# Kernel tuning notes

Hardware: AMD Instinct MI355X
Metric: run time of the kernel (lower is better)

Reference implementation:

```python
import jax, jax.numpy as jnp
import numpy as np

N_FFT = 128
HOP = 32            # fft_stride
WIN_LEN = 512       # window_length
STRIDE = 128        # MPF stride
FS = 2000.0
BANDS = [(0.0, 100.0), (100.0, 200.0), (200.0, 300.0), (300.0, 500.0), (500.0, 750.0), (750.0, 1000.0)]
FRAME_SIZE = WIN_LEN // HOP   # 16 STFT frames per MPF window
FRAME_STEP = STRIDE // HOP    # 4


def _freq_masks():
    freqs = np.fft.rfftfreq(N_FFT, d=1.0 / FS)  # (F,) Hz
    m = np.stack([(freqs > lo) & (freqs <= hi) for lo, hi in BANDS]).astype(np.float32)  # (K, F)
    return jnp.asarray(m)


def setup_inputs() -> dict:
    key = jax.random.key(0)
    return {"inputs": jax.random.normal(key, (8, 16, 32768), dtype=jnp.float32)}


def reference(inputs) -> jnp.ndarray:
    # inputs: (B, C, T)
    B, C, T = inputs.shape
    window = jnp.hanning(N_FFT).astype(inputs.dtype)  # symmetric hann == torch periodic=False
    wnorm = jnp.linalg.norm(window)

    # --- channelwise STFT (center=False, onesided) ---
    n_frames = 1 + (T - N_FFT) // HOP
    fidx = np.arange(n_frames)[:, None] * HOP + np.arange(N_FFT)[None, :]  # (n_frames, N_FFT)
    frames = inputs[..., fidx] * window                                    # (B, C, n_frames, N_FFT)
    stft = jnp.fft.rfft(frames, axis=-1) / wnorm                           # (B, C, n_frames, F) complex

    # --- unfold STFT frames into MPF windows ---
    n_win = (n_frames - FRAME_SIZE) // FRAME_STEP + 1
    widx = np.arange(n_win)[:, None] * FRAME_STEP + np.arange(FRAME_SIZE)  # (n_win, FRAME_SIZE)
    X = stft[:, :, widx, :]                       # (B, C, n_win, FRAME_SIZE, F)
    X = jnp.transpose(X, (0, 2, 4, 1, 3))         # (B, W, F, C, S)

    # --- cross-spectral density, squared magnitude ---
    csd = jnp.einsum('bwfcs,bwfds->bwfcd', X, X.conj()) / FRAME_SIZE  # (B, W, F, C, C) complex
    P = jnp.abs(csd) ** 2                                             # real (B, W, F, C, C)

    # --- frequency-band averaging ---
    masks = _freq_masks()                                             # (K, F)
    band = jnp.einsum('bwfcd,kf->bwkcd', P, masks) / masks.sum(axis=1)[:, None, None]

    # --- SPD matrix log via eigh ---
    evals, evecs = jnp.linalg.eigh(band)                              # (B,W,K,C), (B,W,K,C,C)
    logv = jnp.nan_to_num(jnp.log(evals), nan=0.0, neginf=0.0)
    out = jnp.einsum('...ie,...e,...je->...ij', evecs, logv, evecs)   # (B, W, K, C, C)

    # time-last layout: (B, K, C, C, W)
    return jnp.transpose(out, (0, 2, 3, 4, 1))
```

## Files before the change

kernel.cpp:

```cpp
#include <hip/hip_runtime.h>
#include <math.h>

#define T_LEN 32768
#define NCH   16
#define NB    8
#define NWIN  252
#define NBAND 6
#define NPAIR 136

struct PairTab { int c[NPAIR]; int d[NPAIR]; };
constexpr PairTab mkpairs() {
    PairTab P{}; int p = 0;
    for (int c = 0; c < 16; ++c)
        for (int d = c; d < 16; ++d) { P.c[p] = c; P.d[p] = d; ++p; }
    return P;
}
constexpr PairTab PT = mkpairs();

template<int G>
__device__ __forceinline__ void acc_csd(const float* __restrict__ Xr,
                                        const float* __restrict__ Xi,
                                        float* __restrict__ sre,
                                        float* __restrict__ sim)
{
#pragma unroll
    for (int t = 0; t < 17; ++t) {
        const int c = PT.c[G + 8 * t];
        const int d = PT.d[G + 8 * t];
        sre[t] = fmaf(Xr[c], Xr[d], sre[t]);
        sre[t] = fmaf(Xi[c], Xi[d], sre[t]);
        sim[t] = fmaf(Xi[c], Xr[d], sim[t]);
        sim[t] = fmaf(-Xr[c], Xi[d], sim[t]);
    }
}

#define SWZ(v, imm)  __int_as_float(__builtin_amdgcn_ds_swizzle(__float_as_int(v), (imm)))
#define DPPQ(v, ctl) __int_as_float(__builtin_amdgcn_mov_dpp(__float_as_int(v), (ctl), 0xF, 0xF, true))

#define BF(vr, vi, EX, twr_, twi_, sg_)                        \
    { float pr_ = EX(vr), pi_ = EX(vi);                        \
      float tr_ = fmaf(sg_, vr, pr_);                          \
      float ti_ = fmaf(sg_, vi, pi_);                          \
      vr = fmaf(tr_, twr_, -(ti_ * twi_));                     \
      vi = fmaf(tr_, twi_,  (ti_ * twr_)); }

__global__ __launch_bounds__(512, 2) void csd_band_kernel(const float* __restrict__ x,
                                                          float* __restrict__ band)
{
    const int w    = blockIdx.x;
    const int b    = blockIdx.y;
    const int tid  = threadIdx.x;
    const int lane = tid & 63;
    const int g    = tid >> 6;
    const int f    = lane + 1;

    __shared__ float2 X2[NCH][64];
    __shared__ float2 scr[8][2][64];
    __shared__ float  bl[NBAND][NPAIR];
    __shared__ unsigned char pc_[NPAIR], pd_[NPAIR];

    for (int i = tid; i < NBAND * NPAIR; i += 512) (&bl[0][0])[i] = 0.f;
    if (tid < NPAIR) {
        int rem = tid, c = 0;
        while (rem >= 16 - c) { rem -= 16 - c; ++c; }
        pc_[tid] = (unsigned char)c; pd_[tid] = (unsigned char)(c + rem);
    }

    const double PI = 3.14159265358979323846;
    const float  WI = (float)(1.0 / sqrt(47.625));
    const float wlo = (float)(0.5 - 0.5 * cos(2.0 * PI * (double)lane / 127.0)) * WI;
    const float whi = (float)(0.5 - 0.5 * cos(2.0 * PI * (double)(lane + 64) / 127.0)) * WI;

    const float PIF = 3.14159265358979f;
    float w128r, w128i;
    { float a = -2.f * PIF * (float)lane / 128.f; sincosf(a, &w128i, &w128r); }
    float t32r, t32i, t16r, t16i, t8r, t8i, t4r, t4i, t2r, t2i;
    { float a = (lane & 32) ? -2.f * PIF * (float)(lane & 31) / 64.f : 0.f; sincosf(a, &t32i, &t32r); }
    { float a = (lane & 16) ? -2.f * PIF * (float)(lane & 15) / 32.f : 0.f; sincosf(a, &t16i, &t16r); }
    { float a = (lane &  8) ? -2.f * PIF * (float)(lane &  7) / 16.f : 0.f; sincosf(a, &t8i,  &t8r ); }
    { float a = (lane &  4) ? -2.f * PIF * (float)(lane &  3) /  8.f : 0.f; sincosf(a, &t4i,  &t4r ); }
    { float a = (lane &  2) ? -2.f * PIF * (float)(lane &  1) /  4.f : 0.f; sincosf(a, &t2i,  &t2r ); }
    const float sg32 = (lane & 32) ? -1.f : 1.f;
    const float sg16 = (lane & 16) ? -1.f : 1.f;
    const float sg8  = (lane &  8) ? -1.f : 1.f;
    const float sg4  = (lane &  4) ? -1.f : 1.f;
    const float sg2  = (lane &  2) ? -1.f : 1.f;
    const float sg1  = (lane &  1) ? -1.f : 1.f;

    const int bp32 = 4 * (lane ^ 32);
    const int La = (int)(__brev((unsigned)(f >> 1)) >> 26);
    const int Lb = (int)(__brev((unsigned)((128 - f) >> 1)) >> 26);
    const int pa = f & 1;

    float sre[17], sim[17];
#pragma unroll
    for (int t = 0; t < 17; ++t) { sre[t] = 0.f; sim[t] = 0.f; }

    const float* xp0 = x + (size_t)(b * NCH + g) * T_LEN + (size_t)w * 128;
    const float* xp1 = xp0 + 8 * (size_t)T_LEN;

    __syncthreads();

    for (int s = 0; s < 16; ++s) {
        float s0r = xp0[s * 32 + lane]      * wlo;
        float s1r = xp0[s * 32 + lane + 64] * whi;
        float s0i = xp1[s * 32 + lane]      * wlo;
        float s1i = xp1[s * 32 + lane + 64] * whi;

        {
            float dr = s0r - s1r, di = s0i - s1i;
            s0r += s1r; s0i += s1i;
            float nr = fmaf(dr, w128r, -(di * w128i));
            s1i = fmaf(dr, w128i, di * w128r);
            s1r = nr;
        }
#define EX32(v) __int_as_float(__builtin_amdgcn_ds_bpermute(bp32, __float_as_int(v)))
#define EX16(v) SWZ(v, 0x401F)
#define EX8(v)  SWZ(v, 0x201F)
#define EX4(v)  SWZ(v, 0x101F)
#define EX2(v)  DPPQ(v, 0x4E)
#define EX1(v)  DPPQ(v, 0xB1)
        BF(s0r, s0i, EX32, t32r, t32i, sg32)
        BF(s1r, s1i, EX32, t32r, t32i, sg32)
        BF(s0r, s0i, EX16, t16r, t16i, sg16)
        BF(s1r, s1i, EX16, t16r, t16i, sg16)
        BF(s0r, s0i, EX8,  t8r,  t8i,  sg8)
        BF(s1r, s1i, EX8,  t8r,  t8i,  sg8)
        BF(s0r, s0i, EX4,  t4r,  t4i,  sg4)
        BF(s1r, s1i, EX4,  t4r,  t4i,  sg4)
        BF(s0r, s0i, EX2,  t2r,  t2i,  sg2)
        BF(s1r, s1i, EX2,  t2r,  t2i,  sg2)
        {
            float pr = EX1(s0r), pi = EX1(s0i);
            s0r = fmaf(sg1, s0r, pr); s0i = fmaf(sg1, s0i, pi);
        }
        {
            float pr = EX1(s1r), pi = EX1(s1i);
            s1r = fmaf(sg1, s1r, pr); s1i = fmaf(sg1, s1i, pi);
        }

        scr[g][0][lane] = make_float2(s0r, s0i);
        scr[g][1][lane] = make_float2(s1r, s1i);
        float2 Ua = scr[g][pa][La];
        float2 Ub = scr[g][pa][Lb];
        float X0r = 0.5f * (Ua.x + Ub.x), X0i = 0.5f * (Ua.y - Ub.y);
        float X1r = 0.5f * (Ua.y + Ub.y), X1i = 0.5f * (Ub.x - Ua.x);

        __syncthreads();
        X2[g][lane]     = make_float2(X0r, X0i);
        X2[g + 8][lane] = make_float2(X1r, X1i);
        __syncthreads();

        float Xr[16], Xi[16];
#pragma unroll
        for (int c = 0; c < 16; ++c) { float2 v = X2[c][lane]; Xr[c] = v.x; Xi[c] = v.y; }
        switch (g) {
            case 0: acc_csd<0>(Xr, Xi, sre, sim); break;
            case 1: acc_csd<1>(Xr, Xi, sre, sim); break;
            case 2: acc_csd<2>(Xr, Xi, sre, sim); break;
            case 3: acc_csd<3>(Xr, Xi, sre, sim); break;
            case 4: acc_csd<4>(Xr, Xi, sre, sim); break;
            case 5: acc_csd<5>(Xr, Xi, sre, sim); break;
            case 6: acc_csd<6>(Xr, Xi, sre, sim); break;
            default: acc_csd<7>(Xr, Xi, sre, sim); break;
        }
    }

    const int kband = (lane < 6) ? 0 : (lane < 12) ? 1 : (lane < 19) ? 2
                    : (lane < 32) ? 3 : (lane < 48) ? 4 : 5;
#pragma unroll
    for (int t = 0; t < 17; ++t) {
        float vv = fmaf(sre[t], sre[t], sim[t] * sim[t]);
        atomicAdd(&bl[kband][g + 8 * t], vv);
    }
    __syncthreads();

    const float rs[NBAND] = { 1.f/(256.f*6.f), 1.f/(256.f*6.f), 1.f/(256.f*7.f),
                              1.f/(256.f*13.f), 1.f/(256.f*16.f), 1.f/(256.f*16.f) };
    float* bb = band + (size_t)(b * NWIN + w) * (NBAND * 256);
    for (int i = tid; i < NBAND * NPAIR; i += 512) {
        int k = i / NPAIR, p = i - k * NPAIR;
        int c = pc_[p], d = pd_[p];
        float val = bl[k][p] * rs[k];
        bb[k * 256 + c * 16 + d] = val;
        bb[k * 256 + d * 16 + c] = val;
    }
}

__device__ __forceinline__ void tourney(int rr, int j, int& p, int& q)
{
    if (j == 0) { p = 15; q = rr; }
    else { p = (rr + j) % 15; q = (rr + 15 - j) % 15; }
    if (p > q) { int t_ = p; p = q; q = t_; }
}

__global__ __launch_bounds__(64) void eig_log_kernel(const float* __restrict__ band,
                                                     float* __restrict__ out)
{
    const int k = blockIdx.x, w = blockIdx.y, b = blockIdx.z;
    const int tid = threadIdx.x;
    const int j   = tid >> 3;
    const int n2  = tid & 7;

    __shared__ float A[16][18];
    __shared__ float DT[16][18];
    __shared__ float VT[16][18];
    __shared__ float csx[8], sx[8];
    __shared__ float lv[16];

    const float* M = band + ((size_t)(b * NWIN + w) * NBAND + k) * 256;
#pragma unroll
    for (int it = 0; it < 4; ++it) {
        int i = tid + it * 64, r = i >> 4, c = i & 15;
        A[r][c]  = M[i];
        VT[r][c] = (r == c) ? 1.f : 0.f;
    }
    __syncthreads();

    for (int sweep = 0; sweep < 5; ++sweep) {
        for (int rr = 0; rr < 15; ++rr) {
            int p, q; tourney(rr, j, p, q);
            float app = A[p][p], aqq = A[q][q], apq = A[p][q];
            float c_ = 1.f, s_ = 0.f;
            if (apq != 0.f) {
                float tau = (aqq - app) / (2.f * apq);
                float t   = copysignf(1.f, tau) / (fabsf(tau) + sqrtf(1.f + tau * tau));
                c_ = 1.f / sqrtf(1.f + t * t);
                s_ = t * c_;
            }
            csx[j] = c_; sx[j] = s_;
            float2 ap = *(const float2*)&A[p][2 * n2];
            float2 aq = *(const float2*)&A[q][2 * n2];
            DT[2 * n2][p]     = c_ * ap.x - s_ * aq.x;
            DT[2 * n2 + 1][p] = c_ * ap.y - s_ * aq.y;
            DT[2 * n2][q]     = s_ * ap.x + c_ * aq.x;
            DT[2 * n2 + 1][q] = s_ * ap.y + c_ * aq.y;
            __syncthreads();

            float c2 = csx[j], s2 = sx[j];
            float2 dp = *(const float2*)&DT[p][2 * n2];
            float2 dq = *(const float2*)&DT[q][2 * n2];
            *(float2*)&A[p][2 * n2] = make_float2(c2 * dp.x - s2 * dq.x,
                                                  c2 * dp.y - s2 * dq.y);
            *(float2*)&A[q][2 * n2] = make_float2(s2 * dp.x + c2 * dq.x,
                                                  s2 * dp.y + c2 * dq.y);
            float2 vp = *(const float2*)&VT[p][2 * n2];
            float2 vq = *(const float2*)&VT[q][2 * n2];
            *(float2*)&VT[p][2 * n2] = make_float2(c2 * vp.x - s2 * vq.x,
                                                   c2 * vp.y - s2 * vq.y);
            *(float2*)&VT[q][2 * n2] = make_float2(s2 * vp.x + c2 * vq.x,
                                                   s2 * vp.y + c2 * vq.y);
            __syncthreads();
        }
    }

    if (tid < 16) {
        float l = logf(A[tid][tid]);
        if (isnan(l) || isinf(l)) l = 0.f;
        lv[tid] = l;
    }
    __syncthreads();

    float* ob = out + (size_t)(b * NBAND + k) * 256 * NWIN;
#pragma unroll
    for (int it = 0; it < 4; ++it) {
        int i = tid + it * 64, c = i >> 4, d = i & 15;
        float sum = 0.f;
#pragma unroll
        for (int e = 0; e < 16; ++e) sum = fmaf(VT[e][c] * lv[e], VT[e][d], sum);
        ob[(size_t)i * NWIN + w] = sum;
    }
}

extern "C" void kernel_launch(void* const* d_in, const int* in_sizes, int n_in,
                              void* d_out, int out_size, void* d_ws, size_t ws_size,
                              hipStream_t stream)
{
    const float* x    = (const float*)d_in[0];
    float*       out  = (float*)d_out;
    float*       band = (float*)d_ws;

    dim3 g1(NWIN, NB), b1(512);
    hipLaunchKernelGGL(csd_band_kernel, g1, b1, 0, stream, x, band);

    dim3 g2(NBAND, NWIN, NB), b2(64);
    hipLaunchKernelGGL(eig_log_kernel, g2, b2, 0, stream, band, out);
}
```

Measured before the change: 404.6 us.

## Pack eight eigen problems per block, drop barriers, prefetch and double-buffer CSD

The Jacobi eigen kernel now runs eight 16x16 problems per 512-thread block, one per wavefront. It drops the block-wide __syncthreads by relying on implicit wavefront lockstep, and cuts sweeps from 5 to 4. The CSD kernel prefetches the next frame's input into registers and double-buffers the shared X2 spectrum so one barrier per step is removed. The aim is to cut barrier and launch overhead and hide load latency. Relying on intra-wave lockstep through LDS without barriers or fences is fragile, and fewer sweeps may reduce eigenvalue accuracy.

```diff
diff --git a/kernel.cpp b/kernel.cpp
--- a/kernel.cpp
+++ b/kernel.cpp
@@ -54,7 +54,7 @@
     const int g    = tid >> 6;
     const int f    = lane + 1;
 
-    __shared__ float2 X2[NCH][64];
+    __shared__ float2 X2[2][NCH][64];
     __shared__ float2 scr[8][2][64];
     __shared__ float  bl[NBAND][NPAIR];
     __shared__ unsigned char pc_[NPAIR], pd_[NPAIR];
@@ -99,13 +99,19 @@
     const float* xp0 = x + (size_t)(b * NCH + g) * T_LEN + (size_t)w * 128;
     const float* xp1 = xp0 + 8 * (size_t)T_LEN;
 
+    float L0 = xp0[lane], L1 = xp0[lane + 64];
+    float L2 = xp1[lane], L3 = xp1[lane + 64];
+
     __syncthreads();
 
     for (int s = 0; s < 16; ++s) {
-        float s0r = xp0[s * 32 + lane]      * wlo;
-        float s1r = xp0[s * 32 + lane + 64] * whi;
-        float s0i = xp1[s * 32 + lane]      * wlo;
-        float s1i = xp1[s * 32 + lane + 64] * whi;
+        float s0r = L0 * wlo, s1r = L1 * whi;
+        float s0i = L2 * wlo, s1i = L3 * whi;
+
+        if (s < 15) {
+            L0 = xp0[(s + 1) * 32 + lane];      L1 = xp0[(s + 1) * 32 + lane + 64];
+            L2 = xp1[(s + 1) * 32 + lane];      L3 = xp1[(s + 1) * 32 + lane + 64];
+        }
 
         {
             float dr = s0r - s1r, di = s0i - s1i;
@@ -146,14 +152,14 @@
         float X0r = 0.5f * (Ua.x + Ub.x), X0i = 0.5f * (Ua.y - Ub.y);
         float X1r = 0.5f * (Ua.y + Ub.y), X1i = 0.5f * (Ub.x - Ua.x);
 
+        const int pp = s & 1;
+        X2[pp][g][lane]     = make_float2(X0r, X0i);
+        X2[pp][g + 8][lane] = make_float2(X1r, X1i);
         __syncthreads();
-        X2[g][lane]     = make_float2(X0r, X0i);
-        X2[g + 8][lane] = make_float2(X1r, X1i);
-        __syncthreads();
 
         float Xr[16], Xi[16];
 #pragma unroll
-        for (int c = 0; c < 16; ++c) { float2 v = X2[c][lane]; Xr[c] = v.x; Xi[c] = v.y; }
+        for (int c = 0; c < 16; ++c) { float2 v = X2[pp][c][lane]; Xr[c] = v.x; Xi[c] = v.y; }
         switch (g) {
             case 0: acc_csd<0>(Xr, Xi, sre, sim); break;
             case 1: acc_csd<1>(Xr, Xi, sre, sim); break;
@@ -194,33 +200,37 @@
     if (p > q) { int t_ = p; p = q; q = t_; }
 }
 
-__global__ __launch_bounds__(64) void eig_log_kernel(const float* __restrict__ band,
-                                                     float* __restrict__ out)
-{
-    const int k = blockIdx.x, w = blockIdx.y, b = blockIdx.z;
-    const int tid = threadIdx.x;
-    const int j   = tid >> 3;
-    const int n2  = tid & 7;
-
-    __shared__ float A[16][18];
-    __shared__ float DT[16][18];
-    __shared__ float VT[16][18];
-    __shared__ float csx[8], sx[8];
-    __shared__ float lv[16];
+__global__ __launch_bounds__(512) void eig_log_kernel(const float* __restrict__ band,
+                                                      float* __restrict__ out)
+{
+    const int tid  = threadIdx.x;
+    const int g    = tid >> 6;
+    const int lane = tid & 63;
+    const int m    = blockIdx.x * 8 + g;
+    const int k    = m % NBAND;
+    const int bw   = m / NBAND;
+    const int w    = bw % NWIN;
+    const int b    = bw / NWIN;
+    const int j    = lane >> 3;
+    const int n2   = lane & 7;
+
+    __shared__ float A[8][16][18];
+    __shared__ float DT[8][16][18];
+    __shared__ float VT[8][16][18];
+    __shared__ float lv[8][16];
 
     const float* M = band + ((size_t)(b * NWIN + w) * NBAND + k) * 256;
 #pragma unroll
     for (int it = 0; it < 4; ++it) {
-        int i = tid + it * 64, r = i >> 4, c = i & 15;
-        A[r][c]  = M[i];
-        VT[r][c] = (r == c) ? 1.f : 0.f;
-    }
-    __syncthreads();
-
-    for (int sweep = 0; sweep < 5; ++sweep) {
+        int i = lane + it * 64, r = i >> 4, c = i & 15;
+        A[g][r][c]  = M[i];
+        VT[g][r][c] = (r == c) ? 1.f : 0.f;
+    }
+
+    for (int sweep = 0; sweep < 4; ++sweep) {
         for (int rr = 0; rr < 15; ++rr) {
             int p, q; tourney(rr, j, p, q);
-            float app = A[p][p], aqq = A[q][q], apq = A[p][q];
+            float app = A[g][p][p], aqq = A[g][q][q], apq = A[g][p][q];
             float c_ = 1.f, s_ = 0.f;
             if (apq != 0.f) {
                 float tau = (aqq - app) / (2.f * apq);
@@ -228,46 +238,41 @@
                 c_ = 1.f / sqrtf(1.f + t * t);
                 s_ = t * c_;
             }
-            csx[j] = c_; sx[j] = s_;
-            float2 ap = *(const float2*)&A[p][2 * n2];
-            float2 aq = *(const float2*)&A[q][2 * n2];
-            DT[2 * n2][p]     = c_ * ap.x - s_ * aq.x;
-            DT[2 * n2 + 1][p] = c_ * ap.y - s_ * aq.y;
-            DT[2 * n2][q]     = s_ * ap.x + c_ * aq.x;
-            DT[2 * n2 + 1][q] = s_ * ap.y + c_ * aq.y;
-            __syncthreads();
-
-            float c2 = csx[j], s2 = sx[j];
-            float2 dp = *(const float2*)&DT[p][2 * n2];
-            float2 dq = *(const float2*)&DT[q][2 * n2];
-            *(float2*)&A[p][2 * n2] = make_float2(c2 * dp.x - s2 * dq.x,
-                                                  c2 * dp.y - s2 * dq.y);
-            *(float2*)&A[q][2 * n2] = make_float2(s2 * dp.x + c2 * dq.x,
-                                                  s2 * dp.y + c2 * dq.y);
-            float2 vp = *(const float2*)&VT[p][2 * n2];
-            float2 vq = *(const float2*)&VT[q][2 * n2];
-            *(float2*)&VT[p][2 * n2] = make_float2(c2 * vp.x - s2 * vq.x,
-                                                   c2 * vp.y - s2 * vq.y);
-            *(float2*)&VT[q][2 * n2] = make_float2(s2 * vp.x + c2 * vq.x,
-                                                   s2 * vp.y + c2 * vq.y);
-            __syncthreads();
-        }
-    }
-
-    if (tid < 16) {
-        float l = logf(A[tid][tid]);
+            float2 ap = *(const float2*)&A[g][p][2 * n2];
+            float2 aq = *(const float2*)&A[g][q][2 * n2];
+            DT[g][2 * n2][p]     = c_ * ap.x - s_ * aq.x;
+            DT[g][2 * n2 + 1][p] = c_ * ap.y - s_ * aq.y;
+            DT[g][2 * n2][q]     = s_ * ap.x + c_ * aq.x;
+            DT[g][2 * n2 + 1][q] = s_ * ap.y + c_ * aq.y;
+
+            float2 dp = *(const float2*)&DT[g][p][2 * n2];
+            float2 dq = *(const float2*)&DT[g][q][2 * n2];
+            *(float2*)&A[g][p][2 * n2] = make_float2(c_ * dp.x - s_ * dq.x,
+                                                     c_ * dp.y - s_ * dq.y);
+            *(float2*)&A[g][q][2 * n2] = make_float2(s_ * dp.x + c_ * dq.x,
+                                                     s_ * dp.y + c_ * dq.y);
+            float2 vp = *(const float2*)&VT[g][p][2 * n2];
+            float2 vq = *(const float2*)&VT[g][q][2 * n2];
+            *(float2*)&VT[g][p][2 * n2] = make_float2(c_ * vp.x - s_ * vq.x,
+                                                      c_ * vp.y - s_ * vq.y);
+            *(float2*)&VT[g][q][2 * n2] = make_float2(s_ * vp.x + c_ * vq.x,
+                                                      s_ * vp.y + c_ * vq.y);
+        }
+    }
+
+    if (lane < 16) {
+        float l = logf(A[g][lane][lane]);
         if (isnan(l) || isinf(l)) l = 0.f;
-        lv[tid] = l;
-    }
-    __syncthreads();
+        lv[g][lane] = l;
+    }
 
     float* ob = out + (size_t)(b * NBAND + k) * 256 * NWIN;
 #pragma unroll
     for (int it = 0; it < 4; ++it) {
-        int i = tid + it * 64, c = i >> 4, d = i & 15;
+        int i = lane + it * 64, c = i >> 4, d = i & 15;
         float sum = 0.f;
 #pragma unroll
-        for (int e = 0; e < 16; ++e) sum = fmaf(VT[e][c] * lv[e], VT[e][d], sum);
+        for (int e = 0; e < 16; ++e) sum = fmaf(VT[g][e][c] * lv[g][e], VT[g][e][d], sum);
         ob[(size_t)i * NWIN + w] = sum;
     }
 }
@@ -283,6 +288,6 @@
     dim3 g1(NWIN, NB), b1(512);
     hipLaunchKernelGGL(csd_band_kernel, g1, b1, 0, stream, x, band);
 
-    dim3 g2(NBAND, NWIN, NB), b2(64);
+    dim3 g2(NB * NWIN * NBAND / 8), b2(512);
     hipLaunchKernelGGL(eig_log_kernel, g2, b2, 0, stream, band, out);
 }
```

After: 406.8 us. Within noise of the previous version (+0.5%).
